# Kernel tuning notes

Hardware: AMD Instinct MI355X
Metric: run time of the kernel (lower is better)

Reference implementation:

```python
import jax, jax.numpy as jnp
import numpy as np

B, C, H, W, NP = 4, 512, 32, 32, 2048
NH = 4
EPS = 1e-5


def setup_inputs() -> dict:
    key = jax.random.key(0)
    ks = jax.random.split(key, 12)
    s = 0.02
    d = {}
    d["img_feature"] = jax.random.normal(ks[0], (B, C, H, W), jnp.float32)
    d["point_feature"] = jax.random.normal(ks[1], (B, C, NP), jnp.float32)
    d["mlp_w1"] = jax.random.normal(ks[2], (2 * C, C), jnp.float32) * s
    d["mlp_b1"] = jnp.zeros((2 * C,), jnp.float32)
    d["bn1_gamma"] = jnp.ones((2 * C,), jnp.float32)
    d["bn1_beta"] = jnp.zeros((2 * C,), jnp.float32)
    d["bn1_mean"] = jnp.zeros((2 * C,), jnp.float32)
    d["bn1_var"] = jnp.ones((2 * C,), jnp.float32)
    d["mlp_w2"] = jax.random.normal(ks[3], (C, 2 * C), jnp.float32) * s
    d["mlp_b2"] = jnp.zeros((C,), jnp.float32)
    d["bn2_gamma"] = jnp.ones((C,), jnp.float32)
    d["bn2_beta"] = jnp.zeros((C,), jnp.float32)
    d["bn2_mean"] = jnp.zeros((C,), jnp.float32)
    d["bn2_var"] = jnp.ones((C,), jnp.float32)
    d["attn_qw"] = jax.random.normal(ks[4], (3, C, C), jnp.float32) * s
    d["attn_qb"] = jnp.zeros((3, C), jnp.float32)
    d["attn_kw"] = jax.random.normal(ks[5], (3, C, C), jnp.float32) * s
    d["attn_kb"] = jnp.zeros((3, C), jnp.float32)
    d["attn_vw"] = jax.random.normal(ks[6], (3, C, C), jnp.float32) * s
    d["attn_vb"] = jnp.zeros((3, C), jnp.float32)
    d["attn_ln_g"] = jnp.ones((3, C), jnp.float32)
    d["attn_ln_b"] = jnp.zeros((3, C), jnp.float32)
    return d


def _bn(x, g, b, m, v):  # x: [B, C, N], eval-mode batchnorm over channel dim
    return (x - m[:, None]) * jax.lax.rsqrt(v[:, None] + EPS) * g[:, None] + b[:, None]


def _mlp(x, w1, b1, g1, be1, m1, v1, w2, b2, g2, be2, m2, v2):
    # 1x1 Conv1d == per-position linear over channels
    y = jnp.einsum('oc,bcn->bon', w1, x) + b1[:, None]
    y = jax.nn.relu(_bn(y, g1, be1, m1, v1))
    z = jnp.einsum('oc,bcn->bon', w2, y) + b2[:, None]
    return jax.nn.relu(_bn(z, g2, be2, m2, v2))


def _self_attn(x, qw, qb, kw, kb, vw, vb, lng, lnb):
    # x: [B, S, E]; NOTE: original scales by 1/sqrt(hidden_size), not head_dim
    Bq, S, E = x.shape
    Hd = E // NH
    q = (jnp.einsum('bse,de->bsd', x, qw) + qb).reshape(Bq, S, NH, Hd)
    k = (jnp.einsum('bse,de->bsd', x, kw) + kb).reshape(Bq, S, NH, Hd)
    v = (jnp.einsum('bse,de->bsd', x, vw) + vb).reshape(Bq, S, NH, Hd)
    scores = jnp.einsum('bqhd,bkhd->bhqk', q, k) * (float(E) ** -0.5)
    attn = jax.nn.softmax(scores, axis=-1)
    out = jnp.einsum('bhqk,bkhd->bqhd', attn, v).reshape(Bq, S, E)
    y = out + x
    mu = jnp.mean(y, axis=-1, keepdims=True)
    var = jnp.var(y, axis=-1, keepdims=True)
    return (y - mu) * jax.lax.rsqrt(var + EPS) * lng + lnb


def reference(img_feature, point_feature, mlp_w1, mlp_b1, bn1_gamma, bn1_beta,
              bn1_mean, bn1_var, mlp_w2, mlp_b2, bn2_gamma, bn2_beta, bn2_mean,
              bn2_var, attn_qw, attn_qb, attn_kw, attn_kb, attn_vw, attn_vb,
              attn_ln_g, attn_ln_b):
    b, c, h, w = img_feature.shape
    i_in = img_feature.reshape(b, c, h * w)  # [B, C, N_i]
    mlp_args = (mlp_w1, mlp_b1, bn1_gamma, bn1_beta, bn1_mean, bn1_var,
                mlp_w2, mlp_b2, bn2_gamma, bn2_beta, bn2_mean, bn2_var)
    p_feat = _mlp(point_feature, *mlp_args)  # [B, C, N_p]
    i_feat = _mlp(i_in, *mlp_args)           # [B, C, N_i]
    phi = jnp.einsum('bcp,bci->bpi', p_feat, i_feat) * (float(c) ** -0.5)
    phi_p = jax.nn.softmax(phi, axis=1)   # softmax over points
    phi_i = jax.nn.softmax(phi, axis=-1)  # softmax over image positions
    I_enh = jnp.einsum('bcp,bpi->bci', p_feat, phi_p)  # [B, C, N_i]
    P_enh = jnp.einsum('bci,bpi->bcp', i_feat, phi_i)  # [B, C, N_p]
    att = lambda x, j: _self_attn(x, attn_qw[j], attn_qb[j], attn_kw[j],
                                  attn_kb[j], attn_vw[j], attn_vb[j],
                                  attn_ln_g[j], attn_ln_b[j])
    I = att(jnp.swapaxes(I_enh, 1, 2), 0)  # [B, N_i, C]
    P = att(jnp.swapaxes(P_enh, 1, 2), 1)  # [B, N_p, C]
    joint = jnp.concatenate([P, I], axis=1)  # [B, N_p + N_i, C]
    return att(joint, 2)
```

## Files before the change

kernel.cpp:

```cpp
#include <hip/hip_runtime.h>
#include <math.h>

#define LN_EPS 1e-5f

typedef __attribute__((ext_vector_type(8))) short bf16x8;
typedef __attribute__((ext_vector_type(4))) float f32x4;
typedef unsigned short u16t;

#define GLDS16(g, l) __builtin_amdgcn_global_load_lds( \
    (const __attribute__((address_space(1))) unsigned int*)(g), \
    (__attribute__((address_space(3))) unsigned int*)(l), 16, 0, 0)

__device__ __forceinline__ float b2f(unsigned short h) { return __uint_as_float(((unsigned)h) << 16); }
__device__ __forceinline__ unsigned short f2b(float f) {
  unsigned u = __float_as_uint(f);
  unsigned r = (u + 0x7fffu + ((u >> 16) & 1u)) >> 16;
  return (unsigned short)r;
}
__device__ __forceinline__ float ld(const float* p) { return *p; }
__device__ __forceinline__ float ld(const unsigned short* p) { return b2f(*p); }
__device__ __forceinline__ void st(float* p, float v) { *p = v; }
__device__ __forceinline__ void st(unsigned short* p, float v) { *p = f2b(v); }

__device__ __forceinline__ float bred_sum(float v, float* red) {
  for (int o = 32; o; o >>= 1) v += __shfl_down(v, o, 64);
  int wid = threadIdx.x >> 6;
  __syncthreads();
  if ((threadIdx.x & 63) == 0) red[wid] = v;
  __syncthreads();
  return red[0] + red[1] + red[2] + red[3];
}

__global__ void prep_all(
    const float* __restrict__ w1, const float* __restrict__ w2, const float* __restrict__ vw,
    const float* __restrict__ qw, const float* __restrict__ qb,
    const float* __restrict__ kw, const float* __restrict__ kb,
    const float* __restrict__ b1, const float* __restrict__ g1, const float* __restrict__ be1,
    const float* __restrict__ m1, const float* __restrict__ v1,
    const float* __restrict__ b2, const float* __restrict__ g2, const float* __restrict__ be2,
    const float* __restrict__ m2, const float* __restrict__ v2,
    unsigned short* __restrict__ w1b, unsigned short* __restrict__ w2b,
    unsigned short* __restrict__ vwb, unsigned short* __restrict__ qkw,
    float* __restrict__ qkbias, float* __restrict__ s1, float* __restrict__ f1,
    float* __restrict__ s2, float* __restrict__ f2)
{
  const float scl = 0.044194173824159216f * 1.4426950408889634f;
  int idx = blockIdx.x * 256 + threadIdx.x;
  {
    int j = idx >> 19; int r = idx & 524287; int n = r >> 9; int k = r & 511;
    float v = (n < 512) ? qw[j * 262144 + n * 512 + k] * scl
                        : kw[j * 262144 + (n - 512) * 512 + k];
    qkw[idx] = f2b(v);
  }
  if (idx < 524288) { w1b[idx] = f2b(w1[idx]); w2b[idx] = f2b(w2[idx]); }
  if (idx < 786432) vwb[idx] = f2b(vw[idx]);
  if (idx < 3072) {
    int j = idx >> 10, n = idx & 1023;
    qkbias[idx] = (n < 512) ? qb[j * 512 + n] * scl : kb[j * 512 + n - 512];
  }
  if (idx < 1024) { float s = g1[idx] * rsqrtf(v1[idx] + LN_EPS); s1[idx] = s; f1[idx] = (b1[idx] - m1[idx]) * s + be1[idx]; }
  if (idx < 512)  { float s = g2[idx] * rsqrtf(v2[idx] + LN_EPS); s2[idx] = s; f2[idx] = (b2[idx] - m2[idx]) * s + be2[idx]; }
}

template<typename TS, typename TD>
__global__ __launch_bounds__(256) void transpose_t(const TS* __restrict__ src,
    TD* __restrict__ dst, int R, int Cc, long sS, long sD) {
  __shared__ float t[32][33];
  src += (long)blockIdx.z * sS; dst += (long)blockIdx.z * sD;
  int c0 = blockIdx.x * 32, r0 = blockIdx.y * 32;
  int tx = threadIdx.x & 31, ty = threadIdx.x >> 5;
#pragma unroll
  for (int rr = 0; rr < 32; rr += 8) t[ty + rr][tx] = ld(&src[(long)(r0 + ty + rr) * Cc + c0 + tx]);
  __syncthreads();
#pragma unroll
  for (int rr = 0; rr < 32; rr += 8) st(&dst[(long)(c0 + ty + rr) * R + r0 + tx], t[tx][ty + rr]);
}

template<int PER>
__global__ __launch_bounds__(256) void softmax_k(const float* __restrict__ x,
    unsigned short* __restrict__ y, long bstr) {
  __shared__ float red[4];
  const int L = PER * 256;
  int b = blockIdx.y, r = blockIdx.x, tid = threadIdx.x;
  const float* p = x + (long)b * bstr + (long)r * L;
  unsigned short* o = y + (long)b * bstr + (long)r * L;
  float vals[PER];
  float mx = -1e30f;
#pragma unroll
  for (int t = 0; t < PER; t++) { float v = p[tid + (t << 8)]; vals[t] = v; mx = fmaxf(mx, v); }
  for (int ofs = 32; ofs; ofs >>= 1) mx = fmaxf(mx, __shfl_down(mx, ofs, 64));
  int wid = tid >> 6;
  if ((tid & 63) == 0) red[wid] = mx;
  __syncthreads();
  mx = fmaxf(fmaxf(red[0], red[1]), fmaxf(red[2], red[3]));
  float sm = 0.f;
#pragma unroll
  for (int t = 0; t < PER; t++) { float e = __expf(vals[t] - mx); vals[t] = e; sm += e; }
  sm = bred_sum(sm, red);
  float inv = 1.f / sm;
#pragma unroll
  for (int t = 0; t < PER; t++) o[tid + (t << 8)] = f2b(vals[t] * inv);
}

template<typename TC>
struct GArgs {
  const unsigned short* A; long sA; int lda;
  const unsigned short* B; long sB; int ldb;
  TC* C; long sC; int ldc;
  int M, N, K;
  const float* sc; const float* bi; float cscale; TC* ct;
};

template<int EPI, typename TC>
__device__ __forceinline__ void gemm_body(short* As, short* Bs,
    const unsigned short* __restrict__ A, int lda,
    const unsigned short* __restrict__ B, int ldb,
    TC* __restrict__ C, int ldc, int M, int K,
    const float* sc, const float* bi, float cscale, TC* ct,
    int bm, int bn)
{
  const int tid = threadIdx.x;
  const int lane = tid & 63, wid = tid >> 6;
  const int wm = wid >> 1, wn = wid & 1;
  const int l15 = lane & 15, l4 = lane >> 4, l7 = lane & 7;
  const int srow = lane >> 3;
  f32x4 acc[4][4] = {};
  for (int k0 = 0; k0 < K; k0 += 64) {
#pragma unroll
    for (int i = 0; i < 4; i++) {
      int row = (wid * 4 + i) * 8 + srow;
      int gcol = (l7 ^ (row & 7)) * 8;
      GLDS16(A + (long)(bm + row) * lda + k0 + gcol, &As[(wid * 4 + i) * 512]);
      GLDS16(B + (long)(bn + row) * ldb + k0 + gcol, &Bs[(wid * 4 + i) * 512]);
    }
    __syncthreads();
#pragma unroll
    for (int ks = 0; ks < 2; ks++) {
      bf16x8 af[4], bfr[4];
#pragma unroll
      for (int t = 0; t < 4; t++) {
        int ra = wm * 64 + t * 16 + l15;
        int rb = wn * 64 + t * 16 + l15;
        int ch = (l4 + 4 * ks) ^ (l15 & 7);
        af[t]  = *(const bf16x8*)&As[ra * 64 + ch * 8];
        bfr[t] = *(const bf16x8*)&Bs[rb * 64 + ch * 8];
      }
#pragma unroll
      for (int i = 0; i < 4; i++)
#pragma unroll
        for (int j2 = 0; j2 < 4; j2++)
          acc[i][j2] = __builtin_amdgcn_mfma_f32_16x16x32_bf16(af[i], bfr[j2], acc[i][j2], 0, 0, 0);
    }
    __syncthreads();
  }
#pragma unroll
  for (int i = 0; i < 4; i++) {
#pragma unroll
    for (int j2 = 0; j2 < 4; j2++) {
      int n = bn + wn * 64 + j2 * 16 + l15;
#pragma unroll
      for (int j = 0; j < 4; j++) {
        int m = bm + wm * 64 + i * 16 + l4 * 4 + j;
        float v = acc[i][j2][j];
        if (EPI == 1 || EPI == 6) v = fmaxf(fmaf(v, sc[n], bi[n]), 0.f);
        if (EPI == 2) v *= cscale;
        if (EPI == 3) v += bi[n];
        if (EPI == 4) v += bi[m];
        if (EPI == 5) v *= cscale;
        if (EPI == 5 || EPI == 6) st(&ct[(long)n * M + m], v);
        st(&C[(long)m * ldc + n], v);
      }
    }
  }
}

template<int EPI, typename TC>
__global__ __launch_bounds__(256) void gemm_bf16(GArgs<TC> g) {
  __shared__ short As[128 * 64];
  __shared__ short Bs[128 * 64];
  int b = blockIdx.z;
  gemm_body<EPI, TC>(As, Bs, g.A + (long)b * g.sA, g.lda, g.B + (long)b * g.sB, g.ldb,
      g.C + (long)b * g.sC, g.ldc, g.M, g.K, g.sc, g.bi, g.cscale,
      g.ct ? g.ct + (long)b * g.sC : (TC*)nullptr, blockIdx.y * 128, blockIdx.x * 128);
}

template<int EPI, typename TC>
__global__ __launch_bounds__(256) void gemm_pair(GArgs<TC> g0, GArgs<TC> g1, int mb0, int nb0) {
  __shared__ short As[128 * 64];
  __shared__ short Bs[128 * 64];
  int cfg = blockIdx.z >> 2, b = blockIdx.z & 3;
  if (!cfg && ((int)blockIdx.y >= mb0 || (int)blockIdx.x >= nb0)) return;
  const GArgs<TC>& g = cfg ? g1 : g0;
  gemm_body<EPI, TC>(As, Bs, g.A + (long)b * g.sA, g.lda, g.B + (long)b * g.sB, g.ldb,
      g.C + (long)b * g.sC, g.ldc, g.M, g.K, g.sc, g.bi, g.cscale,
      g.ct ? g.ct + (long)b * g.sC : (TC*)nullptr, blockIdx.y * 128, blockIdx.x * 128);
}

__device__ __forceinline__ void attn_body(short* Ks, short* Vs, short* Ps,
    const unsigned short* __restrict__ qk, const unsigned short* __restrict__ vT,
    unsigned short* __restrict__ out, int S, int qblk, int h, int b)
{
  const int tid = threadIdx.x, lane = tid & 63, wid = tid >> 6;
  const int l15 = lane & 15, l4 = lane >> 4, l7 = l15 & 7;
  const long qkb = (long)b * S * 1024;
  const long vbb = (long)b * 512 * S;
  const long obase = (long)b * S * 512;
  const int qr0 = qblk * 128 + wid * 16;
  const int kR0 = tid >> 4, kC0 = tid & 15;
  const int kR1 = (tid + 512) >> 4, kC1 = tid & 15;
  const int vR0 = tid >> 3, vC0 = tid & 7;
  const int vR1 = (tid + 512) >> 3, vC1 = tid & 7;
  bf16x8 qf[4];
#pragma unroll
  for (int ks = 0; ks < 4; ks++)
    qf[ks] = *(const bf16x8*)(qk + qkb + (long)(qr0 + l15) * 1024 + h * 128 + l4 * 8 + ks * 32);
  bf16x8 onev;
#pragma unroll
  for (int j = 0; j < 8; j++) onev[j] = (short)0x3F80;
  f32x4 O[8] = {};
  f32x4 Ol = {};
  float m_run = -1e30f;
  const int NT = S >> 6;
  int4 kr0, kr1, vr0, vr1;
  auto load_regs = [&](int kt) {
    kr0 = *(const int4*)(qk + qkb + (long)(kt * 64 + kR0) * 1024 + 512 + h * 128 + kC0 * 8);
    kr1 = *(const int4*)(qk + qkb + (long)(kt * 64 + kR1) * 1024 + 512 + h * 128 + kC1 * 8);
    vr0 = *(const int4*)(vT + vbb + (long)(h * 128 + vR0) * S + kt * 64 + vC0 * 8);
    vr1 = *(const int4*)(vT + vbb + (long)(h * 128 + vR1) * S + kt * 64 + vC1 * 8);
  };
  load_regs(0);
  for (int kt = 0; kt < NT; kt++) {
    __syncthreads();
    *(int4*)&Ks[kR0 * 128 + ((kC0 ^ (kR0 & 7)) << 3)] = kr0;
    *(int4*)&Ks[kR1 * 128 + ((kC1 ^ (kR1 & 7)) << 3)] = kr1;
    *(int4*)&Vs[vR0 * 64 + ((vC0 ^ (vR0 & 7)) << 3)] = vr0;
    *(int4*)&Vs[vR1 * 64 + ((vC1 ^ (vR1 & 7)) << 3)] = vr1;
    __syncthreads();
    if (kt + 1 < NT) load_regs(kt + 1);
    f32x4 sacc[4] = {};
    __builtin_amdgcn_s_setprio(1);
#pragma unroll
    for (int f = 0; f < 4; f++) {
      int row = f * 16 + l15;
#pragma unroll
      for (int ks = 0; ks < 4; ks++) {
        bf16x8 kf = *(const bf16x8*)&Ks[row * 128 + (((l4 + 4 * ks) ^ l7) << 3)];
        sacc[f] = __builtin_amdgcn_mfma_f32_16x16x32_bf16(kf, qf[ks], sacc[f], 0, 0, 0);
      }
    }
    __builtin_amdgcn_s_setprio(0);
    float pmax = fmaxf(fmaxf(sacc[0][0], sacc[0][1]), sacc[0][2]);
    pmax = fmaxf(fmaxf(pmax, sacc[0][3]), sacc[1][0]);
    pmax = fmaxf(fmaxf(pmax, sacc[1][1]), sacc[1][2]);
    pmax = fmaxf(fmaxf(pmax, sacc[1][3]), sacc[2][0]);
    pmax = fmaxf(fmaxf(pmax, sacc[2][1]), sacc[2][2]);
    pmax = fmaxf(fmaxf(pmax, sacc[2][3]), sacc[3][0]);
    pmax = fmaxf(fmaxf(pmax, sacc[3][1]), sacc[3][2]);
    pmax = fmaxf(pmax, sacc[3][3]);
    pmax = fmaxf(pmax, __shfl_xor(pmax, 16, 64));
    pmax = fmaxf(pmax, __shfl_xor(pmax, 32, 64));
    if (!__all(pmax - m_run <= 8.f)) {
      float m_new = fmaxf(m_run, pmax);
      float corr = __builtin_exp2f(m_run - m_new);
      m_run = m_new;
      Ol[0] *= corr; Ol[1] *= corr; Ol[2] *= corr; Ol[3] *= corr;
#pragma unroll
      for (int fd = 0; fd < 8; fd++) {
        O[fd][0] *= corr; O[fd][1] *= corr; O[fd][2] *= corr; O[fd][3] *= corr;
      }
    }
#pragma unroll
    for (int f = 0; f < 4; f++) {
      float e0 = __builtin_exp2f(sacc[f][0] - m_run);
      float e1 = __builtin_exp2f(sacc[f][1] - m_run);
      float e2 = __builtin_exp2f(sacc[f][2] - m_run);
      float e3 = __builtin_exp2f(sacc[f][3] - m_run);
      unsigned w0, w1;
      asm("v_cvt_pk_bf16_f32 %0, %1, %2" : "=v"(w0) : "v"(e0), "v"(e1));
      asm("v_cvt_pk_bf16_f32 %0, %1, %2" : "=v"(w1) : "v"(e2), "v"(e3));
      int2 pw; pw.x = (int)w0; pw.y = (int)w1;
      *(int2*)&Ps[wid * 1024 + l15 * 64 + (((2 * f + (l4 >> 1)) ^ l7) << 3) + (l4 & 1) * 4] = pw;
    }
    __builtin_amdgcn_s_setprio(1);
#pragma unroll
    for (int ks = 0; ks < 2; ks++) {
      int pch = ((l4 + 4 * ks) ^ l7) << 3;
      bf16x8 pf = *(const bf16x8*)&Ps[wid * 1024 + l15 * 64 + pch];
      Ol = __builtin_amdgcn_mfma_f32_16x16x32_bf16(onev, pf, Ol, 0, 0, 0);
#pragma unroll
      for (int fd = 0; fd < 8; fd++) {
        bf16x8 vf = *(const bf16x8*)&Vs[(fd * 16 + l15) * 64 + pch];
        O[fd] = __builtin_amdgcn_mfma_f32_16x16x32_bf16(vf, pf, O[fd], 0, 0, 0);
      }
    }
    __builtin_amdgcn_s_setprio(0);
  }
  float inv = 1.f / Ol[0];
  unsigned short* op = out + obase + (long)(qr0 + l15) * 512 + h * 128;
#pragma unroll
  for (int fd = 0; fd < 8; fd++) {
    float a0 = O[fd][0] * inv, a1 = O[fd][1] * inv;
    float a2 = O[fd][2] * inv, a3 = O[fd][3] * inv;
    unsigned wA, wB;
    asm("v_cvt_pk_bf16_f32 %0, %1, %2" : "=v"(wA) : "v"(a0), "v"(a1));
    asm("v_cvt_pk_bf16_f32 %0, %1, %2" : "=v"(wB) : "v"(a2), "v"(a3));
    int2 ov; ov.x = (int)wA; ov.y = (int)wB;
    *(int2*)&op[fd * 16 + l4 * 4] = ov;
  }
}

__global__ __launch_bounds__(512) void attn_flash(
    const unsigned short* __restrict__ qk, const unsigned short* __restrict__ vT,
    unsigned short* __restrict__ out, int S)
{
  __shared__ short Ks[64 * 128];
  __shared__ short Vs[128 * 64];
  __shared__ short Ps[8 * 1024];
  attn_body(Ks, Vs, Ps, qk, vT, out, S, blockIdx.x, blockIdx.y, blockIdx.z);
}

__global__ __launch_bounds__(512) void attn_flash_pair(
    const unsigned short* __restrict__ qk0, const unsigned short* __restrict__ vT0,
    unsigned short* __restrict__ out0, int S0,
    const unsigned short* __restrict__ qk1, const unsigned short* __restrict__ vT1,
    unsigned short* __restrict__ out1, int S1)
{
  __shared__ short Ks[64 * 128];
  __shared__ short Vs[128 * 64];
  __shared__ short Ps[8 * 1024];
  int cfg = blockIdx.z >> 2, b = blockIdx.z & 3;
  const unsigned short* qk = cfg ? qk1 : qk0;
  const unsigned short* vT = cfg ? vT1 : vT0;
  unsigned short* out = cfg ? out1 : out0;
  int S = cfg ? S1 : S0;
  if ((int)blockIdx.x * 128 >= S) return;
  attn_body(Ks, Vs, Ps, qk, vT, out, S, blockIdx.x, blockIdx.y, b);
}

template<typename TD>
__device__ __forceinline__ void add_ln_body(
    const unsigned short* ap, const unsigned short* rp,
    const float* g, const float* bt, TD* dp, float* red)
{
  int tid = threadIdx.x;
  float y0 = b2f(ap[tid]) + b2f(rp[tid]);
  float y1 = b2f(ap[tid + 256]) + b2f(rp[tid + 256]);
  float mu = bred_sum(y0 + y1, red) * (1.f / 512.f);
  float d0 = y0 - mu, d1 = y1 - mu;
  float var = bred_sum(d0 * d0 + d1 * d1, red) * (1.f / 512.f);
  float rsv = rsqrtf(var + LN_EPS);
  st(&dp[tid], d0 * rsv * g[tid] + bt[tid]);
  st(&dp[tid + 256], d1 * rsv * g[tid + 256] + bt[tid + 256]);
}

template<typename TD>
__global__ __launch_bounds__(256) void add_ln(
    const unsigned short* __restrict__ att, const unsigned short* __restrict__ resid,
    const float* __restrict__ g, const float* __restrict__ bt,
    TD* __restrict__ dst, long db, int S)
{
  __shared__ float red[4];
  int b = blockIdx.y, s = blockIdx.x;
  add_ln_body<TD>(att + ((long)b * S + s) * 512, resid + ((long)b * S + s) * 512,
                  g, bt, dst + (long)b * db + (long)s * 512, red);
}

__global__ __launch_bounds__(256) void add_ln_pair(
    const unsigned short* __restrict__ att0, const unsigned short* __restrict__ res0,
    const float* __restrict__ g0, const float* __restrict__ bt0,
    unsigned short* __restrict__ dst0, long db0, int S0,
    const unsigned short* __restrict__ att1, const unsigned short* __restrict__ res1,
    const float* __restrict__ g1, const float* __restrict__ bt1,
    unsigned short* __restrict__ dst1, long db1, int S1)
{
  __shared__ float red[4];
  int b = blockIdx.y, s = blockIdx.x, cfg = blockIdx.z;
  if (cfg == 0) {
    if (s >= S0) return;
    add_ln_body<unsigned short>(att0 + ((long)b * S0 + s) * 512, res0 + ((long)b * S0 + s) * 512,
                                g0, bt0, dst0 + (long)b * db0 + (long)s * 512, red);
  } else {
    add_ln_body<unsigned short>(att1 + ((long)b * S1 + s) * 512, res1 + ((long)b * S1 + s) * 512,
                                g1, bt1, dst1 + (long)b * db1 + (long)s * 512, red);
  }
}

extern "C" void kernel_launch(void* const* d_in, const int* in_sizes, int n_in,
                              void* d_out, int out_size, void* d_ws, size_t ws_size,
                              hipStream_t stream) {
  (void)in_sizes; (void)n_in; (void)out_size; (void)ws_size;
  const float* img = (const float*)d_in[0];
  const float* pts = (const float*)d_in[1];
  const float* w1  = (const float*)d_in[2];
  const float* b1  = (const float*)d_in[3];
  const float* g1  = (const float*)d_in[4];
  const float* be1 = (const float*)d_in[5];
  const float* m1  = (const float*)d_in[6];
  const float* v1  = (const float*)d_in[7];
  const float* w2  = (const float*)d_in[8];
  const float* b2  = (const float*)d_in[9];
  const float* g2  = (const float*)d_in[10];
  const float* be2 = (const float*)d_in[11];
  const float* m2  = (const float*)d_in[12];
  const float* v2  = (const float*)d_in[13];
  const float* qw  = (const float*)d_in[14];
  const float* qb  = (const float*)d_in[15];
  const float* kw  = (const float*)d_in[16];
  const float* kb  = (const float*)d_in[17];
  const float* vw  = (const float*)d_in[18];
  const float* vb  = (const float*)d_in[19];
  const float* lng = (const float*)d_in[20];
  const float* lnb = (const float*)d_in[21];
  float* out = (float*)d_out;
  float* ws  = (float*)d_ws;
  typedef unsigned short u16;

  u16*   xTu   = (u16*)ws;
  float* phi   = ws;
  u16*   y1u   = (u16*)(ws + 8388608);
  float* phiT  = ws + 8388608;
  u16*   featu = (u16*)(ws + 16777216);
  u16*   featTu= (u16*)(ws + 19922944);
  u16*   smI   = (u16*)(ws + 23068672);
  u16*   smPT  = (u16*)(ws + 27262976);
  u16*   Xi    = (u16*)(ws + 31457280);
  u16*   Xp    = (u16*)(ws + 32505856);
  u16*   jointu= (u16*)(ws + 34603008);
  u16*   w1b   = (u16*)(ws + 37748736);
  u16*   w2b   = (u16*)(ws + 38010880);
  u16*   qkwb  = (u16*)(ws + 38273024);
  u16*   vwb   = (u16*)(ws + 39059456);
  float* s1f   = ws + 39452672;
  float* f1f   = s1f + 1024;
  float* s2f   = f1f + 1024;
  float* f2f   = s2f + 512;
  float* qkbf  = ws + 39455744;
  u16*   qk0   = (u16*)ws;
  u16*   qk1   = (u16*)(ws + 2097152);
  u16*   vT0   = (u16*)(ws + 6291456);
  u16*   vT1   = (u16*)(ws + 7340032);
  u16*   out0  = (u16*)(ws + 9437184);
  u16*   out1  = (u16*)(ws + 10485760);
  u16*   qkbu  = (u16*)ws;
  u16*   vTu   = (u16*)(ws + 6291456);
  u16*   attu2 = (u16*)(ws + 9437184);

  dim3 blk(256);
  prep_all<<<dim3(6144), blk, 0, stream>>>(w1, w2, vw, qw, qb, kw, kb,
      b1, g1, be1, m1, v1, b2, g2, be2, m2, v2,
      w1b, w2b, vwb, qkwb, qkbf, s1f, f1f, s2f, f2f);

  transpose_t<float, u16><<<dim3(64, 16, 4), blk, 0, stream>>>(pts, xTu, 512, 2048, 1048576L, 1572864L);
  transpose_t<float, u16><<<dim3(32, 16, 4), blk, 0, stream>>>(img, xTu + 1048576, 512, 1024, 524288L, 1572864L);

  gemm_bf16<1, u16><<<dim3(8, 24, 4), blk, 0, stream>>>(
      GArgs<u16>{xTu, 1572864L, 512, w1b, 0L, 512, y1u, 3145728L, 1024,
                 3072, 1024, 512, s1f, f1f, 0.f, nullptr});
  gemm_bf16<6, u16><<<dim3(4, 24, 4), blk, 0, stream>>>(
      GArgs<u16>{y1u, 3145728L, 1024, w2b, 0L, 1024, featu, 1572864L, 512,
                 3072, 512, 1024, s2f, f2f, 0.f, featTu});
  gemm_bf16<5, float><<<dim3(8, 16, 4), blk, 0, stream>>>(
      GArgs<float>{featu, 1572864L, 512, featu + 1048576, 1572864L, 512, phi, 2097152L, 1024,
                   2048, 1024, 512, nullptr, nullptr, 0.044194173824159216f, phiT});
  softmax_k<4><<<dim3(2048, 4), blk, 0, stream>>>(phi, smI, 2097152L);
  softmax_k<8><<<dim3(1024, 4), blk, 0, stream>>>(phiT, smPT, 2097152L);
  gemm_pair<0, u16><<<dim3(4, 16, 8), blk, 0, stream>>>(
      GArgs<u16>{smPT, 2097152L, 2048, featTu, 1572864L, 3072, Xi, 524288L, 512,
                 1024, 512, 2048, nullptr, nullptr, 0.f, nullptr},
      GArgs<u16>{smI, 2097152L, 1024, featTu + 2048, 1572864L, 3072, Xp, 1048576L, 512,
                 2048, 512, 1024, nullptr, nullptr, 0.f, nullptr}, 8, 4);
  gemm_pair<3, u16><<<dim3(8, 16, 8), blk, 0, stream>>>(
      GArgs<u16>{Xi, 524288L, 512, qkwb, 0L, 512, qk0, 1048576L, 1024,
                 1024, 1024, 512, nullptr, qkbf, 0.f, nullptr},
      GArgs<u16>{Xp, 1048576L, 512, qkwb + 524288, 0L, 512, qk1, 2097152L, 1024,
                 2048, 1024, 512, nullptr, qkbf + 1024, 0.f, nullptr}, 8, 8);
  gemm_pair<4, u16><<<dim3(16, 4, 8), blk, 0, stream>>>(
      GArgs<u16>{vwb, 0L, 512, Xi, 524288L, 512, vT0, 524288L, 1024,
                 512, 1024, 512, nullptr, vb, 0.f, nullptr},
      GArgs<u16>{vwb + 262144, 0L, 512, Xp, 1048576L, 512, vT1, 1048576L, 2048,
                 512, 2048, 512, nullptr, vb + 512, 0.f, nullptr}, 4, 8);
  attn_flash_pair<<<dim3(16, 4, 8), dim3(512), 0, stream>>>(
      qk0, vT0, out0, 1024, qk1, vT1, out1, 2048);
  add_ln_pair<<<dim3(2048, 4, 2), blk, 0, stream>>>(
      out0, Xi, lng, lnb, jointu + 1048576, 1572864L, 1024,
      out1, Xp, lng + 512, lnb + 512, jointu, 1572864L, 2048);
  gemm_bf16<3, u16><<<dim3(8, 24, 4), blk, 0, stream>>>(
      GArgs<u16>{jointu, 1572864L, 512, qkwb + 1048576, 0L, 512, qkbu, 3145728L, 1024,
                 3072, 1024, 512, nullptr, qkbf + 2048, 0.f, nullptr});
  gemm_bf16<4, u16><<<dim3(24, 4, 4), blk, 0, stream>>>(
      GArgs<u16>{vwb + 524288, 0L, 512, jointu, 1572864L, 512, vTu, 1572864L, 3072,
                 512, 3072, 512, nullptr, vb + 1024, 0.f, nullptr});
  attn_flash<<<dim3(24, 4, 4), dim3(512), 0, stream>>>(qkbu, vTu, attu2, 3072);
  add_ln<float><<<dim3(3072, 4), blk, 0, stream>>>(attu2, jointu,
      lng + 1024, lnb + 1024, out, 1572864L, 3072);
}
```

Baseline: 465.3 us.

## Split attention over key range into two halves and merge in add+LayerNorm

The flash-attention kernels for the point branch and the joint branch now split the key/value sequence into two halves, each handled by a separate block. Each block writes unnormalized fp32 partial outputs plus its running max and sum. The following add+LayerNorm kernel merges the two partials with exp2 rescaling before the residual add. The goal is more blocks on the GPU for the long-sequence attention, so it fills the compute units better. The cost is extra fp32 partial-output traffic and a heavier combine step.

```diff
diff --git a/kernel.cpp b/kernel.cpp
--- a/kernel.cpp
+++ b/kernel.cpp
@@ -5,7 +5,6 @@
 
 typedef __attribute__((ext_vector_type(8))) short bf16x8;
 typedef __attribute__((ext_vector_type(4))) float f32x4;
-typedef unsigned short u16t;
 
 #define GLDS16(g, l) __builtin_amdgcn_global_load_lds( \
     (const __attribute__((address_space(1))) unsigned int*)(g), \
@@ -198,7 +197,8 @@
 
 __device__ __forceinline__ void attn_body(short* Ks, short* Vs, short* Ps,
     const unsigned short* __restrict__ qk, const unsigned short* __restrict__ vT,
-    unsigned short* __restrict__ out, int S, int qblk, int h, int b)
+    unsigned short* __restrict__ out, float* __restrict__ pOut, float2* __restrict__ mlrow,
+    int S, int qblk, int h, int b, int kt0, int ktN)
 {
   const int tid = threadIdx.x, lane = tid & 63, wid = tid >> 6;
   const int l15 = lane & 15, l4 = lane >> 4, l7 = l15 & 7;
@@ -220,7 +220,6 @@
   f32x4 O[8] = {};
   f32x4 Ol = {};
   float m_run = -1e30f;
-  const int NT = S >> 6;
   int4 kr0, kr1, vr0, vr1;
   auto load_regs = [&](int kt) {
     kr0 = *(const int4*)(qk + qkb + (long)(kt * 64 + kR0) * 1024 + 512 + h * 128 + kC0 * 8);
@@ -228,15 +227,15 @@
     vr0 = *(const int4*)(vT + vbb + (long)(h * 128 + vR0) * S + kt * 64 + vC0 * 8);
     vr1 = *(const int4*)(vT + vbb + (long)(h * 128 + vR1) * S + kt * 64 + vC1 * 8);
   };
-  load_regs(0);
-  for (int kt = 0; kt < NT; kt++) {
+  load_regs(kt0);
+  for (int kt = kt0; kt < ktN; kt++) {
     __syncthreads();
     *(int4*)&Ks[kR0 * 128 + ((kC0 ^ (kR0 & 7)) << 3)] = kr0;
     *(int4*)&Ks[kR1 * 128 + ((kC1 ^ (kR1 & 7)) << 3)] = kr1;
     *(int4*)&Vs[vR0 * 64 + ((vC0 ^ (vR0 & 7)) << 3)] = vr0;
     *(int4*)&Vs[vR1 * 64 + ((vC1 ^ (vR1 & 7)) << 3)] = vr1;
     __syncthreads();
-    if (kt + 1 < NT) load_regs(kt + 1);
+    if (kt + 1 < ktN) load_regs(kt + 1);
     f32x4 sacc[4] = {};
     __builtin_amdgcn_s_setprio(1);
 #pragma unroll
@@ -295,46 +294,62 @@
     }
     __builtin_amdgcn_s_setprio(0);
   }
-  float inv = 1.f / Ol[0];
-  unsigned short* op = out + obase + (long)(qr0 + l15) * 512 + h * 128;
-#pragma unroll
-  for (int fd = 0; fd < 8; fd++) {
-    float a0 = O[fd][0] * inv, a1 = O[fd][1] * inv;
-    float a2 = O[fd][2] * inv, a3 = O[fd][3] * inv;
-    unsigned wA, wB;
-    asm("v_cvt_pk_bf16_f32 %0, %1, %2" : "=v"(wA) : "v"(a0), "v"(a1));
-    asm("v_cvt_pk_bf16_f32 %0, %1, %2" : "=v"(wB) : "v"(a2), "v"(a3));
-    int2 ov; ov.x = (int)wA; ov.y = (int)wB;
-    *(int2*)&op[fd * 16 + l4 * 4] = ov;
-  }
-}
-
-__global__ __launch_bounds__(512) void attn_flash(
+  if (pOut) {
+    float* pp = pOut + obase + (long)(qr0 + l15) * 512 + h * 128;
+#pragma unroll
+    for (int fd = 0; fd < 8; fd++) *(f32x4*)&pp[fd * 16 + l4 * 4] = O[fd];
+    if (l4 == 0) mlrow[qr0 + l15] = make_float2(m_run, Ol[0]);
+  } else {
+    float inv = 1.f / Ol[0];
+    unsigned short* op = out + obase + (long)(qr0 + l15) * 512 + h * 128;
+#pragma unroll
+    for (int fd = 0; fd < 8; fd++) {
+      float a0 = O[fd][0] * inv, a1 = O[fd][1] * inv;
+      float a2 = O[fd][2] * inv, a3 = O[fd][3] * inv;
+      unsigned wA, wB;
+      asm("v_cvt_pk_bf16_f32 %0, %1, %2" : "=v"(wA) : "v"(a0), "v"(a1));
+      asm("v_cvt_pk_bf16_f32 %0, %1, %2" : "=v"(wB) : "v"(a2), "v"(a3));
+      int2 ov; ov.x = (int)wA; ov.y = (int)wB;
+      *(int2*)&op[fd * 16 + l4 * 4] = ov;
+    }
+  }
+}
+
+__global__ __launch_bounds__(512) void attn_flash_split(
     const unsigned short* __restrict__ qk, const unsigned short* __restrict__ vT,
-    unsigned short* __restrict__ out, int S)
+    float* __restrict__ P0, float* __restrict__ P1, float2* __restrict__ ml, int S)
 {
   __shared__ short Ks[64 * 128];
   __shared__ short Vs[128 * 64];
   __shared__ short Ps[8 * 1024];
-  attn_body(Ks, Vs, Ps, qk, vT, out, S, blockIdx.x, blockIdx.y, blockIdx.z);
+  int split = blockIdx.z >> 2, b = blockIdx.z & 3;
+  int half = (S >> 6) >> 1;
+  int kt0 = split * half, ktN = kt0 + half;
+  float* P = split ? P1 : P0;
+  float2* mlrow = ml + (((long)split * 4 + b) * 4 + blockIdx.y) * S;
+  attn_body(Ks, Vs, Ps, qk, vT, nullptr, P, mlrow, S, blockIdx.x, blockIdx.y, b, kt0, ktN);
 }
 
 __global__ __launch_bounds__(512) void attn_flash_pair(
     const unsigned short* __restrict__ qk0, const unsigned short* __restrict__ vT0,
-    unsigned short* __restrict__ out0, int S0,
+    unsigned short* __restrict__ out0,
     const unsigned short* __restrict__ qk1, const unsigned short* __restrict__ vT1,
-    unsigned short* __restrict__ out1, int S1)
+    float* __restrict__ P0, float* __restrict__ P1, float2* __restrict__ ml)
 {
   __shared__ short Ks[64 * 128];
   __shared__ short Vs[128 * 64];
   __shared__ short Ps[8 * 1024];
   int cfg = blockIdx.z >> 2, b = blockIdx.z & 3;
-  const unsigned short* qk = cfg ? qk1 : qk0;
-  const unsigned short* vT = cfg ? vT1 : vT0;
-  unsigned short* out = cfg ? out1 : out0;
-  int S = cfg ? S1 : S0;
-  if ((int)blockIdx.x * 128 >= S) return;
-  attn_body(Ks, Vs, Ps, qk, vT, out, S, blockIdx.x, blockIdx.y, b);
+  if (cfg == 0) {
+    if ((int)blockIdx.x >= 8) return;
+    attn_body(Ks, Vs, Ps, qk0, vT0, out0, nullptr, nullptr, 1024, blockIdx.x, blockIdx.y, b, 0, 16);
+  } else {
+    int split = cfg - 1;
+    float* P = split ? P1 : P0;
+    float2* mlrow = ml + (((long)split * 4 + b) * 4 + blockIdx.y) * 2048;
+    attn_body(Ks, Vs, Ps, qk1, vT1, nullptr, P, mlrow, 2048, blockIdx.x, blockIdx.y, b,
+              split * 16, split * 16 + 16);
+  }
 }
 
 template<typename TD>
@@ -354,35 +369,65 @@
 }
 
 template<typename TD>
-__global__ __launch_bounds__(256) void add_ln(
-    const unsigned short* __restrict__ att, const unsigned short* __restrict__ resid,
-    const float* __restrict__ g, const float* __restrict__ bt,
-    TD* __restrict__ dst, long db, int S)
-{
-  __shared__ float red[4];
-  int b = blockIdx.y, s = blockIdx.x;
-  add_ln_body<TD>(att + ((long)b * S + s) * 512, resid + ((long)b * S + s) * 512,
-                  g, bt, dst + (long)b * db + (long)s * 512, red);
-}
-
-__global__ __launch_bounds__(256) void add_ln_pair(
+__device__ __forceinline__ void add_ln_comb_body(
+    const float* __restrict__ p0, const float* __restrict__ p1,
+    const float2* __restrict__ ml, int S, int b, int s,
+    const unsigned short* rp, const float* g, const float* bt, TD* dp, float* red)
+{
+  int tid = threadIdx.x;
+  long base = ((long)b * S + s) * 512;
+  float y[2];
+#pragma unroll
+  for (int t = 0; t < 2; t++) {
+    int col = tid + t * 256;
+    int h = col >> 7;
+    float2 a = ml[(((long)0 + b) * 4 + h) * S + s];
+    float2 c = ml[(((long)4 + b) * 4 + h) * S + s];
+    float M = fmaxf(a.x, c.x);
+    float w0 = __builtin_exp2f(a.x - M), w1 = __builtin_exp2f(c.x - M);
+    float inv = 1.f / (a.y * w0 + c.y * w1);
+    y[t] = (p0[base + col] * w0 + p1[base + col] * w1) * inv + b2f(rp[col]);
+  }
+  float mu = bred_sum(y[0] + y[1], red) * (1.f / 512.f);
+  float d0 = y[0] - mu, d1 = y[1] - mu;
+  float var = bred_sum(d0 * d0 + d1 * d1, red) * (1.f / 512.f);
+  float rsv = rsqrtf(var + LN_EPS);
+  st(&dp[tid], d0 * rsv * g[tid] + bt[tid]);
+  st(&dp[tid + 256], d1 * rsv * g[tid + 256] + bt[tid + 256]);
+}
+
+__global__ __launch_bounds__(256) void add_ln_pair2(
     const unsigned short* __restrict__ att0, const unsigned short* __restrict__ res0,
     const float* __restrict__ g0, const float* __restrict__ bt0,
-    unsigned short* __restrict__ dst0, long db0, int S0,
-    const unsigned short* __restrict__ att1, const unsigned short* __restrict__ res1,
+    unsigned short* __restrict__ dst0, long db0,
+    const float* __restrict__ P0, const float* __restrict__ P1,
+    const float2* __restrict__ ml, const unsigned short* __restrict__ res1,
     const float* __restrict__ g1, const float* __restrict__ bt1,
-    unsigned short* __restrict__ dst1, long db1, int S1)
+    unsigned short* __restrict__ dst1, long db1)
 {
   __shared__ float red[4];
   int b = blockIdx.y, s = blockIdx.x, cfg = blockIdx.z;
   if (cfg == 0) {
-    if (s >= S0) return;
-    add_ln_body<unsigned short>(att0 + ((long)b * S0 + s) * 512, res0 + ((long)b * S0 + s) * 512,
+    if (s >= 1024) return;
+    add_ln_body<unsigned short>(att0 + ((long)b * 1024 + s) * 512, res0 + ((long)b * 1024 + s) * 512,
                                 g0, bt0, dst0 + (long)b * db0 + (long)s * 512, red);
   } else {
-    add_ln_body<unsigned short>(att1 + ((long)b * S1 + s) * 512, res1 + ((long)b * S1 + s) * 512,
-                                g1, bt1, dst1 + (long)b * db1 + (long)s * 512, red);
-  }
+    add_ln_comb_body<unsigned short>(P0, P1, ml, 2048, b, s,
+                                     res1 + ((long)b * 2048 + s) * 512,
+                                     g1, bt1, dst1 + (long)b * db1 + (long)s * 512, red);
+  }
+}
+
+__global__ __launch_bounds__(256) void add_ln_comb(
+    const float* __restrict__ P0, const float* __restrict__ P1,
+    const float2* __restrict__ ml, const unsigned short* __restrict__ resid,
+    const float* __restrict__ g, const float* __restrict__ bt,
+    float* __restrict__ dst, long db, int S)
+{
+  __shared__ float red[4];
+  int b = blockIdx.y, s = blockIdx.x;
+  add_ln_comb_body<float>(P0, P1, ml, S, b, s, resid + ((long)b * S + s) * 512,
+                          g, bt, dst + (long)b * db + (long)s * 512, red);
 }
 
 extern "C" void kernel_launch(void* const* d_in, const int* in_sizes, int n_in,
@@ -440,10 +485,14 @@
   u16*   vT0   = (u16*)(ws + 6291456);
   u16*   vT1   = (u16*)(ws + 7340032);
   u16*   out0  = (u16*)(ws + 9437184);
-  u16*   out1  = (u16*)(ws + 10485760);
+  float* P0a1  = ws + 10485760;
+  float* P1a1  = ws + 14680064;
+  float2* ml1  = (float2*)(ws + 18874368);
   u16*   qkbu  = (u16*)ws;
   u16*   vTu   = (u16*)(ws + 6291456);
-  u16*   attu2 = (u16*)(ws + 9437184);
+  float* P0a2  = ws + 9437184;
+  float* P1a2  = ws + 15728640;
+  float2* ml2  = (float2*)(ws + 22020096);
 
   dim3 blk(256);
   prep_all<<<dim3(6144), blk, 0, stream>>>(w1, w2, vw, qw, qb, kw, kb,
@@ -479,18 +528,18 @@
                  512, 1024, 512, nullptr, vb, 0.f, nullptr},
       GArgs<u16>{vwb + 262144, 0L, 512, Xp, 1048576L, 512, vT1, 1048576L, 2048,
                  512, 2048, 512, nullptr, vb + 512, 0.f, nullptr}, 4, 8);
-  attn_flash_pair<<<dim3(16, 4, 8), dim3(512), 0, stream>>>(
-      qk0, vT0, out0, 1024, qk1, vT1, out1, 2048);
-  add_ln_pair<<<dim3(2048, 4, 2), blk, 0, stream>>>(
-      out0, Xi, lng, lnb, jointu + 1048576, 1572864L, 1024,
-      out1, Xp, lng + 512, lnb + 512, jointu, 1572864L, 2048);
+  attn_flash_pair<<<dim3(16, 4, 12), dim3(512), 0, stream>>>(
+      qk0, vT0, out0, qk1, vT1, P0a1, P1a1, ml1);
+  add_ln_pair2<<<dim3(2048, 4, 2), blk, 0, stream>>>(
+      out0, Xi, lng, lnb, jointu + 1048576, 1572864L,
+      P0a1, P1a1, ml1, Xp, lng + 512, lnb + 512, jointu, 1572864L);
   gemm_bf16<3, u16><<<dim3(8, 24, 4), blk, 0, stream>>>(
       GArgs<u16>{jointu, 1572864L, 512, qkwb + 1048576, 0L, 512, qkbu, 3145728L, 1024,
                  3072, 1024, 512, nullptr, qkbf + 2048, 0.f, nullptr});
   gemm_bf16<4, u16><<<dim3(24, 4, 4), blk, 0, stream>>>(
       GArgs<u16>{vwb + 524288, 0L, 512, jointu, 1572864L, 512, vTu, 1572864L, 3072,
                  512, 3072, 512, nullptr, vb + 1024, 0.f, nullptr});
-  attn_flash<<<dim3(24, 4, 4), dim3(512), 0, stream>>>(qkbu, vTu, attu2, 3072);
-  add_ln<float><<<dim3(3072, 4), blk, 0, stream>>>(attu2, jointu,
+  attn_flash_split<<<dim3(24, 4, 8), dim3(512), 0, stream>>>(qkbu, vTu, P0a2, P1a2, ml2, 3072);
+  add_ln_comb<<<dim3(3072, 4), blk, 0, stream>>>(P0a2, P1a2, ml2, jointu,
       lng + 1024, lnb + 1024, out, 1572864L, 3072);
 }
```

Measured after the change: 460.5 us. About the same (-1.0%).
